# Performance work log

Hardware: AMD Instinct MI355X
Metric: run time of the kernel (lower is better)

## Reference

```python
import jax, jax.numpy as jnp
import numpy as np

BN_EPS = 1e-5

def _conv1x1(x, W, b):
    # x: (B,C,H,W), W: (O,C) -> (B,O,H,W)
    return jnp.einsum('oc,bchw->bohw', W, x) + b[None, :, None, None]

def setup_inputs() -> dict:
    key = jax.random.key(0)
    ks = jax.random.split(key, 6)
    B, C, H, W = 4, 256, 64, 64
    cq = C // 8
    x  = jax.random.normal(ks[0], (B, C, H, W), jnp.float32)
    Wq = jax.random.normal(ks[1], (cq, C), jnp.float32) * (1.0 / np.sqrt(C))
    Wk = jax.random.normal(ks[2], (cq, C), jnp.float32) * (1.0 / np.sqrt(C))
    Wv = jax.random.normal(ks[3], (C, C), jnp.float32) * (1.0 / np.sqrt(C))
    Wo = jax.random.normal(ks[4], (C, C, 3, 3), jnp.float32) * (1.0 / np.sqrt(C * 9))
    return {
        'x': x,
        'Wq': Wq, 'bq': jnp.zeros((cq,), jnp.float32),
        'Wk': Wk, 'bk': jnp.zeros((cq,), jnp.float32),
        'Wv': Wv, 'bv': jnp.zeros((C,), jnp.float32),
        'Wo': Wo, 'bo': jnp.zeros((C,), jnp.float32),
        'bn_gamma': jnp.ones((C,), jnp.float32),
        'bn_beta':  jnp.zeros((C,), jnp.float32),
        'bn_mean':  jnp.zeros((C,), jnp.float32),
        'bn_var':   jnp.ones((C,), jnp.float32),
    }

def reference(x, Wq, bq, Wk, bk, Wv, bv, Wo, bo, bn_gamma, bn_beta, bn_mean, bn_var):
    B, C, H, W = x.shape
    cq = Wq.shape[0]
    N = H * W
    q = _conv1x1(x, Wq, bq).reshape(B, cq, N)   # (B,cq,N)
    k = _conv1x1(x, Wk, bk).reshape(B, cq, N)   # (B,cq,N)
    v = _conv1x1(x, Wv, bv).reshape(B, C, N)    # (B,C,N)
    scale = cq ** (-0.5)
    attn = jnp.einsum('bcn,bcm->bnm', q, k) * scale   # (B,N,N)
    attn = jax.nn.softmax(attn, axis=-1)
    out = jnp.einsum('bnm,bcm->bcn', attn, v).reshape(B, C, H, W)
    # conv_output: 3x3 conv + BN (inference stats) + ReLU
    out = jax.lax.conv_general_dilated(
        out, Wo, window_strides=(1, 1), padding=((1, 1), (1, 1)),
        dimension_numbers=('NCHW', 'OIHW', 'NCHW')) + bo[None, :, None, None]
    inv = bn_gamma * jax.lax.rsqrt(bn_var + BN_EPS)
    out = out * inv[None, :, None, None] + (bn_beta - bn_mean * inv)[None, :, None, None]
    out = jax.nn.relu(out)
    return out + x
```

## Files before the change

### kernel.cpp

```cpp
#include <hip/hip_runtime.h>
#include <hip/hip_bf16.h>
#include <math.h>

#define N_TOK 4096

typedef __attribute__((ext_vector_type(8))) short short8;
typedef __attribute__((ext_vector_type(4))) float f32x4;

#define MFMA16(a, b, c) __builtin_amdgcn_mfma_f32_16x16x32_bf16(a, b, c, 0, 0, 0)

__device__ inline unsigned pack_bf16x2(float a, float b) {
    __hip_bfloat16 ha = __float2bfloat16(a), hb = __float2bfloat16(b);
    unsigned short ua = *(unsigned short*)&ha, ub = *(unsigned short*)&hb;
    return (unsigned)ua | ((unsigned)ub << 16);
}

__device__ inline float bf2f(unsigned short u) {
    unsigned v = ((unsigned)u) << 16;
    union { unsigned u; float f; } cv; cv.u = v; return cv.f;
}

__device__ inline int swz4(int h, int row) { return (h ^ row ^ (row >> 2)) & 3; }

#define SCK 0.25506974748975505f

__global__ __launch_bounds__(256) void xt_prep_kernel(
    const float* __restrict__ x, __hip_bfloat16* __restrict__ xt)
{
    __shared__ __hip_bfloat16 tl[64][72];
    int blk = blockIdx.x;
    int cg = blk & 3, ng = (blk >> 2) & 63, b = blk >> 8;
    int n0 = ng * 64, c0 = cg * 64;
    int t = threadIdx.x;
    int cr = t >> 4, part = t & 15;
#pragma unroll
    for (int rep = 0; rep < 4; ++rep) {
        int c = rep * 16 + cr;
        float4 v4 = *(const float4*)&x[((size_t)(b * 256 + c0 + c)) * N_TOK + n0 + part * 4];
        tl[part * 4 + 0][c] = __float2bfloat16(v4.x);
        tl[part * 4 + 1][c] = __float2bfloat16(v4.y);
        tl[part * 4 + 2][c] = __float2bfloat16(v4.z);
        tl[part * 4 + 3][c] = __float2bfloat16(v4.w);
    }
    __syncthreads();
    int n = t >> 2, g = t & 3;
    uint4 u0 = *(uint4*)&tl[n][g * 16];
    uint4 u1 = *(uint4*)&tl[n][g * 16 + 8];
    __hip_bfloat16* dst = &xt[((size_t)(b * N_TOK + n0 + n)) * 256 + c0 + g * 16];
    *(uint4*)dst = u0;
    *(uint4*)&dst[8] = u1;
}

__global__ __launch_bounds__(256) void w_prep_kernel(
    const float* __restrict__ Wo, const float* __restrict__ Wq,
    const float* __restrict__ Wk, const float* __restrict__ Wv,
    __hip_bfloat16* __restrict__ Wt, __hip_bfloat16* __restrict__ Wqk,
    __hip_bfloat16* __restrict__ Wvb)
{
    int blk = blockIdx.x, t = threadIdx.x;
    if (blk < 256) {
        const float* src = &Wo[(size_t)(blk * 256 + t) * 9];
#pragma unroll
        for (int tap = 0; tap < 9; ++tap)
            Wt[(size_t)(tap * 256 + blk) * 256 + t] = __float2bfloat16(src[tap]);
    } else if (blk < 260) {
        int r0 = (blk - 256) * 64;
        for (int r = r0; r < r0 + 64; ++r)
            Wvb[r * 256 + t] = __float2bfloat16(Wv[r * 256 + t]);
    } else {
        for (int r = 0; r < 32; ++r) {
            Wqk[r * 256 + t]        = __float2bfloat16(Wq[r * 256 + t] * SCK);
            Wqk[(r + 32) * 256 + t] = __float2bfloat16(Wk[r * 256 + t]);
        }
    }
}

__global__ __launch_bounds__(256) void qk_mfma_kernel(
    const __hip_bfloat16* __restrict__ xt, const __hip_bfloat16* __restrict__ Wqk,
    const float* __restrict__ bq, const float* __restrict__ bk,
    __hip_bfloat16* __restrict__ qg, __hip_bfloat16* __restrict__ kg)
{
    int blk = blockIdx.x;
    int b = blk >> 6, n0 = (blk & 63) * 64;
    int t = threadIdx.x, w = t >> 6, lane = t & 63;
    int l15 = lane & 15, l4 = lane >> 4;
    int n = n0 + w * 16 + l15;

    f32x4 zf = {0.f, 0.f, 0.f, 0.f};
    f32x4 acc[4];
#pragma unroll
    for (int m = 0; m < 4; ++m) acc[m] = zf;

    const __hip_bfloat16* xrow = &xt[((size_t)(b * N_TOK + n)) * 256];
    for (int k0 = 0; k0 < 256; k0 += 32) {
        short8 bfr = *(const short8*)&xrow[k0 + l4 * 8];
#pragma unroll
        for (int m = 0; m < 4; ++m) {
            short8 af = *(const short8*)&Wqk[(size_t)(m * 16 + l15) * 256 + k0 + l4 * 8];
            acc[m] = MFMA16(af, bfr, acc[m]);
        }
    }
    f32x4 bq0 = *(const f32x4*)&bq[l4 * 4];
    f32x4 bq1 = *(const f32x4*)&bq[16 + l4 * 4];
    f32x4 bk0 = *(const f32x4*)&bk[l4 * 4];
    f32x4 bk1 = *(const f32x4*)&bk[16 + l4 * 4];
    size_t obase = (size_t)(b * N_TOK + n) * 32;
    uint2 u;
    u.x = pack_bf16x2(acc[0][0] + bq0[0] * SCK, acc[0][1] + bq0[1] * SCK);
    u.y = pack_bf16x2(acc[0][2] + bq0[2] * SCK, acc[0][3] + bq0[3] * SCK);
    *(uint2*)&qg[obase + l4 * 4] = u;
    u.x = pack_bf16x2(acc[1][0] + bq1[0] * SCK, acc[1][1] + bq1[1] * SCK);
    u.y = pack_bf16x2(acc[1][2] + bq1[2] * SCK, acc[1][3] + bq1[3] * SCK);
    *(uint2*)&qg[obase + 16 + l4 * 4] = u;
    u.x = pack_bf16x2(acc[2][0] + bk0[0], acc[2][1] + bk0[1]);
    u.y = pack_bf16x2(acc[2][2] + bk0[2], acc[2][3] + bk0[3]);
    *(uint2*)&kg[obase + l4 * 4] = u;
    u.x = pack_bf16x2(acc[3][0] + bk1[0], acc[3][1] + bk1[1]);
    u.y = pack_bf16x2(acc[3][2] + bk1[2], acc[3][3] + bk1[3]);
    *(uint2*)&kg[obase + 16 + l4 * 4] = u;
}

__global__ __launch_bounds__(256) void v_mfma_kernel(
    const __hip_bfloat16* __restrict__ xt, const __hip_bfloat16* __restrict__ Wvb,
    const float* __restrict__ bv, __hip_bfloat16* __restrict__ vg)
{
    int blk = blockIdx.x;
    int b = blk >> 7, ch = (blk >> 6) & 1, n0 = (blk & 63) * 64;
    int c0 = ch * 128;
    int t = threadIdx.x, w = t >> 6, lane = t & 63;
    int l15 = lane & 15, l4 = lane >> 4;
    int n = n0 + w * 16 + l15;

    f32x4 zf = {0.f, 0.f, 0.f, 0.f};
    f32x4 acc[8];
#pragma unroll
    for (int m = 0; m < 8; ++m) acc[m] = zf;

    const __hip_bfloat16* xrow = &xt[((size_t)(b * N_TOK + n)) * 256];
    for (int k0 = 0; k0 < 256; k0 += 32) {
        short8 bfr = *(const short8*)&xrow[k0 + l4 * 8];
#pragma unroll
        for (int m = 0; m < 8; ++m) {
            short8 af = *(const short8*)&Wvb[(size_t)(c0 + m * 16 + l15) * 256 + k0 + l4 * 8];
            acc[m] = MFMA16(af, bfr, acc[m]);
        }
    }
#pragma unroll
    for (int m = 0; m < 8; ++m) {
        int cb = c0 + m * 16 + l4 * 4;
        f32x4 bvv = *(const f32x4*)&bv[cb];
#pragma unroll
        for (int r = 0; r < 4; ++r)
            vg[((size_t)(b * 256 + cb + r)) * N_TOK + n] = __float2bfloat16(acc[m][r] + bvv[r]);
    }
}

__global__ __launch_bounds__(256, 2) void flash_kernel(
    const __hip_bfloat16* __restrict__ qg, const __hip_bfloat16* __restrict__ kg,
    const __hip_bfloat16* __restrict__ vg,
    __hip_bfloat16* __restrict__ ph0, __hip_bfloat16* __restrict__ ph1,
    float* __restrict__ Lh)
{
    __shared__ __hip_bfloat16 v_lds[2][128 * 64];
    __shared__ __hip_bfloat16 k_lds[2][64 * 32];
    __shared__ __hip_bfloat16 p_lds[4][32 * 64];

    int blk = blockIdx.x;
    int work = (blk & 7) * 64 + (blk >> 3);
    int g = work >> 6;
    int kh = g >> 2, cs = (g >> 1) & 1, bl = g & 1;
    int rem = work & 63;
    int b = ((rem >> 5) << 1) | bl;
    int qgp = rem & 31;
    int t = threadIdx.x, w = t >> 6, lane = t & 63;
    int l15 = lane & 15, l4 = lane >> 4;
    int qw = qgp * 128 + w * 32;

    short8 qf[2];
#pragma unroll
    for (int qs = 0; qs < 2; ++qs)
        qf[qs] = *(const short8*)&qg[((size_t)(b * N_TOK + qw + qs * 16 + l15)) * 32 + l4 * 8];

    f32x4 zf = {0.f, 0.f, 0.f, 0.f};
    f32x4 acc[2][8];
#pragma unroll
    for (int qs = 0; qs < 2; ++qs)
#pragma unroll
        for (int ct = 0; ct < 8; ++ct) acc[qs][ct] = zf;
    float Lr[2] = {0.f, 0.f};

    int vc  = t >> 1;
    int kb4 = (t & 1) * 4;
    int kr  = t >> 2;
    int kch = t & 3;

    const __hip_bfloat16* vrow  = &vg[((size_t)(b * 256 + cs * 128 + vc)) * N_TOK + kh * 2048];
    const __hip_bfloat16* kbase = &kg[((size_t)(b * N_TOK + kh * 2048)) * 32];

    uint4 vp[4], kp;

#pragma unroll
    for (int j = 0; j < 4; ++j)
        vp[j] = *(const uint4*)&vrow[(kb4 + j) * 8];
    kp = *(const uint4*)&kbase[kr * 32 + kch * 8];
#pragma unroll
    for (int j = 0; j < 4; ++j)
        *(uint4*)&v_lds[0][vc * 64 + (((2 * (kb4 + j)) ^ (vc & 14)) << 2)] = vp[j];
    *(uint4*)&k_lds[0][kr * 32 + swz4(kch, kr) * 8] = kp;
    __syncthreads();

    int buf = 0;
    for (int it = 0; it < 32; ++it) {
        int nm0 = it * 64 + 64;
        bool more = (it < 31);
        if (more) {
#pragma unroll
            for (int j = 0; j < 4; ++j)
                vp[j] = *(const uint4*)&vrow[nm0 + (kb4 + j) * 8];
            kp = *(const uint4*)&kbase[(size_t)(nm0 + kr) * 32 + kch * 8];
        }

        short8 kf[4];
#pragma unroll
        for (int kt = 0; kt < 4; ++kt) {
            int row = kt * 16 + l15;
            kf[kt] = *(const short8*)&k_lds[buf][row * 32 + swz4(l4, row) * 8];
        }
        f32x4 sf[2][4];
#pragma unroll
        for (int qs = 0; qs < 2; ++qs)
#pragma unroll
            for (int kt = 0; kt < 4; ++kt)
                sf[qs][kt] = MFMA16(kf[kt], qf[qs], zf);

#pragma unroll
        for (int qs = 0; qs < 2; ++qs) {
            int prow = qs * 16 + l15;
#pragma unroll
            for (int kt = 0; kt < 4; ++kt) {
                float p0 = exp2f(sf[qs][kt][0]);
                float p1 = exp2f(sf[qs][kt][1]);
                float p2 = exp2f(sf[qs][kt][2]);
                float p3 = exp2f(sf[qs][kt][3]);
                Lr[qs] += (p0 + p1) + (p2 + p3);
                uint2 u;
                u.x = pack_bf16x2(p0, p1);
                u.y = pack_bf16x2(p2, p3);
                *(uint2*)&p_lds[w][prow * 64 + (((kt * 4 + l4) ^ (l15 & 14)) << 2)] = u;
            }
        }

#pragma unroll
        for (int ks = 0; ks < 2; ++ks) {
            short8 pb[2];
#pragma unroll
            for (int qs = 0; qs < 2; ++qs)
                pb[qs] = *(const short8*)&p_lds[w][(qs * 16 + l15) * 64 +
                         (((ks * 8 + l4 * 2) ^ (l15 & 14)) << 2)];
#pragma unroll
            for (int ct = 0; ct < 8; ++ct) {
                int cr = ct * 16 + l15;
                short8 vf = *(const short8*)&v_lds[buf][cr * 64 +
                           (((ks * 8 + l4 * 2) ^ (cr & 14)) << 2)];
                acc[0][ct] = MFMA16(vf, pb[0], acc[0][ct]);
                acc[1][ct] = MFMA16(vf, pb[1], acc[1][ct]);
            }
        }

        if (more) {
#pragma unroll
            for (int j = 0; j < 4; ++j)
                *(uint4*)&v_lds[buf ^ 1][vc * 64 + (((2 * (kb4 + j)) ^ (vc & 14)) << 2)] = vp[j];
            *(uint4*)&k_lds[buf ^ 1][kr * 32 + swz4(kch, kr) * 8] = kp;
            buf ^= 1;
        }
        __syncthreads();
    }

#pragma unroll
    for (int qs = 0; qs < 2; ++qs) {
        float L = Lr[qs];
        L += __shfl_xor(L, 16);
        L += __shfl_xor(L, 32);
        int nq = qw + qs * 16 + l15;
        if (cs == 0 && l4 == 0)
            Lh[kh * 16384 + b * 4096 + nq] = L;
        __hip_bfloat16* pdst = kh ? ph1 : ph0;
        size_t pix = (size_t)(b * N_TOK + nq);
#pragma unroll
        for (int ct = 0; ct < 8; ++ct) {
            int cl = cs * 128 + ct * 16 + l4 * 4;
            uint2 u;
            u.x = pack_bf16x2(acc[qs][ct][0], acc[qs][ct][1]);
            u.y = pack_bf16x2(acc[qs][ct][2], acc[qs][ct][3]);
            *(uint2*)&pdst[pix * 256 + cl] = u;
        }
    }
}

__global__ __launch_bounds__(256) void linv_kernel(
    const float* __restrict__ Lh, float* __restrict__ Linv)
{
    int i = blockIdx.x * 256 + threadIdx.x;
    Linv[i] = 1.f / (Lh[i] + Lh[16384 + i]);
}

__global__ __launch_bounds__(256) void conv_mfma_kernel(
    const __hip_bfloat16* __restrict__ ph0, const __hip_bfloat16* __restrict__ ph1,
    const float* __restrict__ Linv, const __hip_bfloat16* __restrict__ Wt,
    const float* __restrict__ bo,  const float* __restrict__ gamma,
    const float* __restrict__ beta, const float* __restrict__ mean,
    const float* __restrict__ var, const float* __restrict__ x,
    float* __restrict__ out)
{
    __shared__ __hip_bfloat16 in_lds[180 * 32];
    __shared__ __hip_bfloat16 wt_lds[9 * 64 * 32];

    int blk = blockIdx.x;
    int sp = blk & 31, ob = (blk >> 5) & 3, b = blk >> 7;
    int y0 = (sp >> 2) * 8, x0 = (sp & 3) * 16;
    int o0 = ob * 64;
    int t = threadIdx.x;
    int w = t >> 6, lane = t & 63;
    int l15 = lane & 15, l4 = lane >> 4;

    f32x4 zf = {0.f, 0.f, 0.f, 0.f};
    f32x4 acc[4][2];
#pragma unroll
    for (int m = 0; m < 4; ++m)
#pragma unroll
        for (int n = 0; n < 2; ++n) acc[m][n] = zf;

    for (int cc = 0; cc < 256; cc += 32) {
        __syncthreads();
        for (int jj = t; jj < 720; jj += 256) {
            int pix = jj >> 2, h = jj & 3;
            int iy = pix / 18, ix = pix - iy * 18;
            int gy = y0 - 1 + iy, gx = x0 - 1 + ix;
            uint4 val = {0u, 0u, 0u, 0u};
            if (gy >= 0 && gy < 64 && gx >= 0 && gx < 64) {
                int bn = b * 4096 + gy * 64 + gx;
                float inv = Linv[bn];
                size_t e = (size_t)bn * 256 + cc + h * 8;
                uint4 a  = *(const uint4*)&ph0[e];
                uint4 b4 = *(const uint4*)&ph1[e];
                const unsigned* ap = (const unsigned*)&a;
                const unsigned* bp = (const unsigned*)&b4;
                unsigned* vpn = (unsigned*)&val;
#pragma unroll
                for (int j = 0; j < 4; ++j) {
                    float lo = (bf2f((unsigned short)(ap[j] & 0xffff)) +
                                bf2f((unsigned short)(bp[j] & 0xffff))) * inv;
                    float hi = (bf2f((unsigned short)(ap[j] >> 16)) +
                                bf2f((unsigned short)(bp[j] >> 16))) * inv;
                    vpn[j] = pack_bf16x2(lo, hi);
                }
            }
            *(uint4*)&in_lds[pix * 32 + swz4(h, pix) * 8] = val;
        }
        for (int jj = t; jj < 2304; jj += 256) {
            int tap = jj >> 8, rem = jj & 255;
            int o = rem >> 2, h = rem & 3;
            uint4 wv = *(const uint4*)&Wt[((size_t)(tap * 256 + o0 + o)) * 256 + cc + h * 8];
            *(uint4*)&wt_lds[tap * 2048 + o * 32 + swz4(h, o) * 8] = wv;
        }
        __syncthreads();

#pragma unroll
        for (int ky = 0; ky < 3; ++ky) {
#pragma unroll
            for (int kx = 0; kx < 3; ++kx) {
                int tap = ky * 3 + kx;
                short8 af[4];
#pragma unroll
                for (int m = 0; m < 4; ++m) {
                    int orow = m * 16 + l15;
                    af[m] = *(const short8*)&wt_lds[tap * 2048 + orow * 32 + swz4(l4, orow) * 8];
                }
#pragma unroll
                for (int ntw = 0; ntw < 2; ++ntw) {
                    int yy = w * 2 + ntw;
                    int p = (yy + ky) * 18 + kx + l15;
                    short8 bfr = *(const short8*)&in_lds[p * 32 + swz4(l4, p) * 8];
#pragma unroll
                    for (int m = 0; m < 4; ++m)
                        acc[m][ntw] = MFMA16(af[m], bfr, acc[m][ntw]);
                }
            }
        }
    }

#pragma unroll
    for (int m = 0; m < 4; ++m) {
#pragma unroll
        for (int r = 0; r < 4; ++r) {
            int oc = o0 + m * 16 + l4 * 4 + r;
            float inv = gamma[oc] * rsqrtf(var[oc] + 1e-5f);
            float sh  = (bo[oc] - mean[oc]) * inv + beta[oc];
#pragma unroll
            for (int ntw = 0; ntw < 2; ++ntw) {
                int gy = y0 + w * 2 + ntw, gx = x0 + l15;
                size_t idx = (size_t)(b * 256 + oc) * 4096 + (size_t)gy * 64 + gx;
                float yv = acc[m][ntw][r] * inv + sh;
                yv = fmaxf(yv, 0.f);
                out[idx] = yv + x[idx];
            }
        }
    }
}

extern "C" void kernel_launch(void* const* d_in, const int* in_sizes, int n_in,
                              void* d_out, int out_size, void* d_ws, size_t ws_size,
                              hipStream_t stream)
{
    const float* x  = (const float*)d_in[0];
    const float* Wq = (const float*)d_in[1];
    const float* bq = (const float*)d_in[2];
    const float* Wk = (const float*)d_in[3];
    const float* bk = (const float*)d_in[4];
    const float* Wv = (const float*)d_in[5];
    const float* bv = (const float*)d_in[6];
    const float* Wo = (const float*)d_in[7];
    const float* bo = (const float*)d_in[8];
    const float* gm = (const float*)d_in[9];
    const float* bt = (const float*)d_in[10];
    const float* mn = (const float*)d_in[11];
    const float* vr = (const float*)d_in[12];
    float* out = (float*)d_out;

    char* wsb = (char*)d_ws;
    __hip_bfloat16* qg  = (__hip_bfloat16*)(wsb);
    __hip_bfloat16* kg  = (__hip_bfloat16*)(wsb + (1u  << 20));
    __hip_bfloat16* vg  = (__hip_bfloat16*)(wsb + (2u  << 20));
    __hip_bfloat16* att = (__hip_bfloat16*)(wsb + (10u << 20));
    __hip_bfloat16* Wt  = (__hip_bfloat16*)(wsb + (18u << 20));
    __hip_bfloat16* xt  = (__hip_bfloat16*)(wsb + (20u << 20));
    __hip_bfloat16* Wqk = (__hip_bfloat16*)(wsb + (28u << 20));
    __hip_bfloat16* Wvb = (__hip_bfloat16*)(wsb + (28u << 20) + 65536);
    float*          Lh  = (float*)(wsb + (28u << 20) + 262144);
    float*          Linv= (float*)(wsb + (28u << 20) + 393216);

    __hip_bfloat16* ph0 = xt;
    __hip_bfloat16* ph1 = att;

    w_prep_kernel  <<<261,  256, 0, stream>>>(Wo, Wq, Wk, Wv, Wt, Wqk, Wvb);
    xt_prep_kernel <<<1024, 256, 0, stream>>>(x, xt);
    qk_mfma_kernel <<<256,  256, 0, stream>>>(xt, Wqk, bq, bk, qg, kg);
    v_mfma_kernel  <<<512,  256, 0, stream>>>(xt, Wvb, bv, vg);
    flash_kernel   <<<512,  256, 0, stream>>>(qg, kg, vg, ph0, ph1, Lh);
    linv_kernel    <<<64,   256, 0, stream>>>(Lh, Linv);
    conv_mfma_kernel<<<512, 256, 0, stream>>>(ph0, ph1, Linv, Wt, bo, gm, bt, mn, vr, x, out);
}
```

Before: 160.6 us.

## Split flash attention keys three ways and load K fragments directly into registers

```diff
diff --git a/kernel.cpp b/kernel.cpp
--- a/kernel.cpp
+++ b/kernel.cpp
@@ -155,23 +155,22 @@
     }
 }
 
-__global__ __launch_bounds__(256, 2) void flash_kernel(
+__global__ __launch_bounds__(256, 3) void flash_kernel(
     const __hip_bfloat16* __restrict__ qg, const __hip_bfloat16* __restrict__ kg,
     const __hip_bfloat16* __restrict__ vg,
     __hip_bfloat16* __restrict__ ph0, __hip_bfloat16* __restrict__ ph1,
-    float* __restrict__ Lh)
+    __hip_bfloat16* __restrict__ ph2, float* __restrict__ Lh)
 {
     __shared__ __hip_bfloat16 v_lds[2][128 * 64];
-    __shared__ __hip_bfloat16 k_lds[2][64 * 32];
     __shared__ __hip_bfloat16 p_lds[4][32 * 64];
 
     int blk = blockIdx.x;
-    int work = (blk & 7) * 64 + (blk >> 3);
-    int g = work >> 6;
-    int kh = g >> 2, cs = (g >> 1) & 1, bl = g & 1;
-    int rem = work & 63;
-    int b = ((rem >> 5) << 1) | bl;
-    int qgp = rem & 31;
+    int work = (blk & 7) * 96 + (blk >> 3);
+    int kh = work >> 8;
+    int rem = work & 255;
+    int cs = rem >> 7, b = (rem >> 5) & 3, qgp = rem & 31;
+    int koff  = (kh == 0) ? 0 : (kh == 1 ? 1408 : 2752);
+    int iters = (kh == 0) ? 22 : 21;
     int t = threadIdx.x, w = t >> 6, lane = t & 63;
     int l15 = lane & 15, l4 = lane >> 4;
     int qw = qgp * 128 + w * 32;
@@ -191,47 +190,43 @@
 
     int vc  = t >> 1;
     int kb4 = (t & 1) * 4;
-    int kr  = t >> 2;
-    int kch = t & 3;
-
-    const __hip_bfloat16* vrow  = &vg[((size_t)(b * 256 + cs * 128 + vc)) * N_TOK + kh * 2048];
-    const __hip_bfloat16* kbase = &kg[((size_t)(b * N_TOK + kh * 2048)) * 32];
-
-    uint4 vp[4], kp;
+
+    const __hip_bfloat16* vrow  = &vg[((size_t)(b * 256 + cs * 128 + vc)) * N_TOK + koff];
+    const __hip_bfloat16* kbase = &kg[((size_t)(b * N_TOK + koff)) * 32];
+
+    uint4 vp[4];
+    short8 kfr[4], kfn[4];
 
 #pragma unroll
     for (int j = 0; j < 4; ++j)
         vp[j] = *(const uint4*)&vrow[(kb4 + j) * 8];
-    kp = *(const uint4*)&kbase[kr * 32 + kch * 8];
+#pragma unroll
+    for (int kt = 0; kt < 4; ++kt)
+        kfr[kt] = *(const short8*)&kbase[(kt * 16 + l15) * 32 + l4 * 8];
 #pragma unroll
     for (int j = 0; j < 4; ++j)
         *(uint4*)&v_lds[0][vc * 64 + (((2 * (kb4 + j)) ^ (vc & 14)) << 2)] = vp[j];
-    *(uint4*)&k_lds[0][kr * 32 + swz4(kch, kr) * 8] = kp;
     __syncthreads();
 
     int buf = 0;
-    for (int it = 0; it < 32; ++it) {
+    for (int it = 0; it < iters; ++it) {
         int nm0 = it * 64 + 64;
-        bool more = (it < 31);
+        bool more = (it < iters - 1);
         if (more) {
 #pragma unroll
             for (int j = 0; j < 4; ++j)
                 vp[j] = *(const uint4*)&vrow[nm0 + (kb4 + j) * 8];
-            kp = *(const uint4*)&kbase[(size_t)(nm0 + kr) * 32 + kch * 8];
-        }
-
-        short8 kf[4];
-#pragma unroll
-        for (int kt = 0; kt < 4; ++kt) {
-            int row = kt * 16 + l15;
-            kf[kt] = *(const short8*)&k_lds[buf][row * 32 + swz4(l4, row) * 8];
-        }
+#pragma unroll
+            for (int kt = 0; kt < 4; ++kt)
+                kfn[kt] = *(const short8*)&kbase[(size_t)(nm0 + kt * 16 + l15) * 32 + l4 * 8];
+        }
+
         f32x4 sf[2][4];
 #pragma unroll
         for (int qs = 0; qs < 2; ++qs)
 #pragma unroll
             for (int kt = 0; kt < 4; ++kt)
-                sf[qs][kt] = MFMA16(kf[kt], qf[qs], zf);
+                sf[qs][kt] = MFMA16(kfr[kt], qf[qs], zf);
 
 #pragma unroll
         for (int qs = 0; qs < 2; ++qs) {
@@ -271,7 +266,8 @@
 #pragma unroll
             for (int j = 0; j < 4; ++j)
                 *(uint4*)&v_lds[buf ^ 1][vc * 64 + (((2 * (kb4 + j)) ^ (vc & 14)) << 2)] = vp[j];
-            *(uint4*)&k_lds[buf ^ 1][kr * 32 + swz4(kch, kr) * 8] = kp;
+#pragma unroll
+            for (int kt = 0; kt < 4; ++kt) kfr[kt] = kfn[kt];
             buf ^= 1;
         }
         __syncthreads();
@@ -285,7 +281,7 @@
         int nq = qw + qs * 16 + l15;
         if (cs == 0 && l4 == 0)
             Lh[kh * 16384 + b * 4096 + nq] = L;
-        __hip_bfloat16* pdst = kh ? ph1 : ph0;
+        __hip_bfloat16* pdst = (kh == 0) ? ph0 : (kh == 1 ? ph1 : ph2);
         size_t pix = (size_t)(b * N_TOK + nq);
 #pragma unroll
         for (int ct = 0; ct < 8; ++ct) {
@@ -302,12 +298,13 @@
     const float* __restrict__ Lh, float* __restrict__ Linv)
 {
     int i = blockIdx.x * 256 + threadIdx.x;
-    Linv[i] = 1.f / (Lh[i] + Lh[16384 + i]);
+    Linv[i] = 1.f / (Lh[i] + Lh[16384 + i] + Lh[32768 + i]);
 }
 
 __global__ __launch_bounds__(256) void conv_mfma_kernel(
     const __hip_bfloat16* __restrict__ ph0, const __hip_bfloat16* __restrict__ ph1,
-    const float* __restrict__ Linv, const __hip_bfloat16* __restrict__ Wt,
+    const __hip_bfloat16* __restrict__ ph2, const float* __restrict__ Linv,
+    const __hip_bfloat16* __restrict__ Wt,
     const float* __restrict__ bo,  const float* __restrict__ gamma,
     const float* __restrict__ beta, const float* __restrict__ mean,
     const float* __restrict__ var, const float* __restrict__ x,
@@ -344,15 +341,19 @@
                 size_t e = (size_t)bn * 256 + cc + h * 8;
                 uint4 a  = *(const uint4*)&ph0[e];
                 uint4 b4 = *(const uint4*)&ph1[e];
+                uint4 c4 = *(const uint4*)&ph2[e];
                 const unsigned* ap = (const unsigned*)&a;
                 const unsigned* bp = (const unsigned*)&b4;
+                const unsigned* cp = (const unsigned*)&c4;
                 unsigned* vpn = (unsigned*)&val;
 #pragma unroll
                 for (int j = 0; j < 4; ++j) {
                     float lo = (bf2f((unsigned short)(ap[j] & 0xffff)) +
-                                bf2f((unsigned short)(bp[j] & 0xffff))) * inv;
+                                bf2f((unsigned short)(bp[j] & 0xffff)) +
+                                bf2f((unsigned short)(cp[j] & 0xffff))) * inv;
                     float hi = (bf2f((unsigned short)(ap[j] >> 16)) +
-                                bf2f((unsigned short)(bp[j] >> 16))) * inv;
+                                bf2f((unsigned short)(bp[j] >> 16)) +
+                                bf2f((unsigned short)(cp[j] >> 16))) * inv;
                     vpn[j] = pack_bf16x2(lo, hi);
                 }
             }
@@ -438,7 +439,8 @@
     __hip_bfloat16* Wqk = (__hip_bfloat16*)(wsb + (28u << 20));
     __hip_bfloat16* Wvb = (__hip_bfloat16*)(wsb + (28u << 20) + 65536);
     float*          Lh  = (float*)(wsb + (28u << 20) + 262144);
-    float*          Linv= (float*)(wsb + (28u << 20) + 393216);
+    float*          Linv= (float*)(wsb + (28u << 20) + 458752);
+    __hip_bfloat16* ph2 = (__hip_bfloat16*)(wsb + (29u << 20));
 
     __hip_bfloat16* ph0 = xt;
     __hip_bfloat16* ph1 = att;
@@ -447,7 +449,7 @@
     xt_prep_kernel <<<1024, 256, 0, stream>>>(x, xt);
     qk_mfma_kernel <<<256,  256, 0, stream>>>(xt, Wqk, bq, bk, qg, kg);
     v_mfma_kernel  <<<512,  256, 0, stream>>>(xt, Wvb, bv, vg);
-    flash_kernel   <<<512,  256, 0, stream>>>(qg, kg, vg, ph0, ph1, Lh);
+    flash_kernel   <<<768,  256, 0, stream>>>(qg, kg, vg, ph0, ph1, ph2, Lh);
     linv_kernel    <<<64,   256, 0, stream>>>(Lh, Linv);
-    conv_mfma_kernel<<<512, 256, 0, stream>>>(ph0, ph1, Linv, Wt, bo, gm, bt, mn, vr, x, out);
-}
+    conv_mfma_kernel<<<512, 256, 0, stream>>>(ph0, ph1, ph2, Linv, Wt, bo, gm, bt, mn, vr, x, out);
+}
```

Measured after the change: 179.0 us. 11.4% more time.

## Fuse x transpose, QK and V projections into one kernel; inline L reciprocal

Applied to the files above, without the earlier changes.

```diff
diff --git a/kernel.cpp b/kernel.cpp
--- a/kernel.cpp
+++ b/kernel.cpp
@@ -23,33 +23,6 @@
 __device__ inline int swz4(int h, int row) { return (h ^ row ^ (row >> 2)) & 3; }
 
 #define SCK 0.25506974748975505f
-
-__global__ __launch_bounds__(256) void xt_prep_kernel(
-    const float* __restrict__ x, __hip_bfloat16* __restrict__ xt)
-{
-    __shared__ __hip_bfloat16 tl[64][72];
-    int blk = blockIdx.x;
-    int cg = blk & 3, ng = (blk >> 2) & 63, b = blk >> 8;
-    int n0 = ng * 64, c0 = cg * 64;
-    int t = threadIdx.x;
-    int cr = t >> 4, part = t & 15;
-#pragma unroll
-    for (int rep = 0; rep < 4; ++rep) {
-        int c = rep * 16 + cr;
-        float4 v4 = *(const float4*)&x[((size_t)(b * 256 + c0 + c)) * N_TOK + n0 + part * 4];
-        tl[part * 4 + 0][c] = __float2bfloat16(v4.x);
-        tl[part * 4 + 1][c] = __float2bfloat16(v4.y);
-        tl[part * 4 + 2][c] = __float2bfloat16(v4.z);
-        tl[part * 4 + 3][c] = __float2bfloat16(v4.w);
-    }
-    __syncthreads();
-    int n = t >> 2, g = t & 3;
-    uint4 u0 = *(uint4*)&tl[n][g * 16];
-    uint4 u1 = *(uint4*)&tl[n][g * 16 + 8];
-    __hip_bfloat16* dst = &xt[((size_t)(b * N_TOK + n0 + n)) * 256 + c0 + g * 16];
-    *(uint4*)dst = u0;
-    *(uint4*)&dst[8] = u1;
-}
 
 __global__ __launch_bounds__(256) void w_prep_kernel(
     const float* __restrict__ Wo, const float* __restrict__ Wq,
@@ -75,11 +48,15 @@
     }
 }
 
-__global__ __launch_bounds__(256) void qk_mfma_kernel(
-    const __hip_bfloat16* __restrict__ xt, const __hip_bfloat16* __restrict__ Wqk,
+__global__ __launch_bounds__(256) void qkv_kernel(
+    const float* __restrict__ x,
+    const __hip_bfloat16* __restrict__ Wqk, const __hip_bfloat16* __restrict__ Wvb,
     const float* __restrict__ bq, const float* __restrict__ bk,
-    __hip_bfloat16* __restrict__ qg, __hip_bfloat16* __restrict__ kg)
+    const float* __restrict__ bv,
+    __hip_bfloat16* __restrict__ qg, __hip_bfloat16* __restrict__ kg,
+    __hip_bfloat16* __restrict__ vg)
 {
+    __shared__ __hip_bfloat16 tl[64][72];
     int blk = blockIdx.x;
     int b = blk >> 6, n0 = (blk & 63) * 64;
     int t = threadIdx.x, w = t >> 6, lane = t & 63;
@@ -87,71 +64,69 @@
     int n = n0 + w * 16 + l15;
 
     f32x4 zf = {0.f, 0.f, 0.f, 0.f};
-    f32x4 acc[4];
-#pragma unroll
-    for (int m = 0; m < 4; ++m) acc[m] = zf;
-
-    const __hip_bfloat16* xrow = &xt[((size_t)(b * N_TOK + n)) * 256];
-    for (int k0 = 0; k0 < 256; k0 += 32) {
-        short8 bfr = *(const short8*)&xrow[k0 + l4 * 8];
-#pragma unroll
-        for (int m = 0; m < 4; ++m) {
-            short8 af = *(const short8*)&Wqk[(size_t)(m * 16 + l15) * 256 + k0 + l4 * 8];
-            acc[m] = MFMA16(af, bfr, acc[m]);
-        }
-    }
+    f32x4 aqk[4], av[16];
+#pragma unroll
+    for (int m = 0; m < 4; ++m) aqk[m] = zf;
+#pragma unroll
+    for (int m = 0; m < 16; ++m) av[m] = zf;
+
+    int cr = t >> 4, part = t & 15;
+
+    for (int cc = 0; cc < 256; cc += 64) {
+        __syncthreads();
+#pragma unroll
+        for (int rep = 0; rep < 4; ++rep) {
+            int c = rep * 16 + cr;
+            float4 v4 = *(const float4*)&x[((size_t)(b * 256 + cc + c)) * N_TOK + n0 + part * 4];
+            tl[part * 4 + 0][c] = __float2bfloat16(v4.x);
+            tl[part * 4 + 1][c] = __float2bfloat16(v4.y);
+            tl[part * 4 + 2][c] = __float2bfloat16(v4.z);
+            tl[part * 4 + 3][c] = __float2bfloat16(v4.w);
+        }
+        __syncthreads();
+#pragma unroll
+        for (int kk = 0; kk < 2; ++kk) {
+            int k0 = cc + kk * 32;
+            short8 bfr = *(const short8*)&tl[w * 16 + l15][kk * 32 + l4 * 8];
+#pragma unroll
+            for (int m = 0; m < 4; ++m) {
+                short8 af = *(const short8*)&Wqk[(size_t)(m * 16 + l15) * 256 + k0 + l4 * 8];
+                aqk[m] = MFMA16(af, bfr, aqk[m]);
+            }
+#pragma unroll
+            for (int m = 0; m < 16; ++m) {
+                short8 af = *(const short8*)&Wvb[(size_t)(m * 16 + l15) * 256 + k0 + l4 * 8];
+                av[m] = MFMA16(af, bfr, av[m]);
+            }
+        }
+    }
+
     f32x4 bq0 = *(const f32x4*)&bq[l4 * 4];
     f32x4 bq1 = *(const f32x4*)&bq[16 + l4 * 4];
     f32x4 bk0 = *(const f32x4*)&bk[l4 * 4];
     f32x4 bk1 = *(const f32x4*)&bk[16 + l4 * 4];
     size_t obase = (size_t)(b * N_TOK + n) * 32;
     uint2 u;
-    u.x = pack_bf16x2(acc[0][0] + bq0[0] * SCK, acc[0][1] + bq0[1] * SCK);
-    u.y = pack_bf16x2(acc[0][2] + bq0[2] * SCK, acc[0][3] + bq0[3] * SCK);
+    u.x = pack_bf16x2(aqk[0][0] + bq0[0] * SCK, aqk[0][1] + bq0[1] * SCK);
+    u.y = pack_bf16x2(aqk[0][2] + bq0[2] * SCK, aqk[0][3] + bq0[3] * SCK);
     *(uint2*)&qg[obase + l4 * 4] = u;
-    u.x = pack_bf16x2(acc[1][0] + bq1[0] * SCK, acc[1][1] + bq1[1] * SCK);
-    u.y = pack_bf16x2(acc[1][2] + bq1[2] * SCK, acc[1][3] + bq1[3] * SCK);
+    u.x = pack_bf16x2(aqk[1][0] + bq1[0] * SCK, aqk[1][1] + bq1[1] * SCK);
+    u.y = pack_bf16x2(aqk[1][2] + bq1[2] * SCK, aqk[1][3] + bq1[3] * SCK);
     *(uint2*)&qg[obase + 16 + l4 * 4] = u;
-    u.x = pack_bf16x2(acc[2][0] + bk0[0], acc[2][1] + bk0[1]);
-    u.y = pack_bf16x2(acc[2][2] + bk0[2], acc[2][3] + bk0[3]);
+    u.x = pack_bf16x2(aqk[2][0] + bk0[0], aqk[2][1] + bk0[1]);
+    u.y = pack_bf16x2(aqk[2][2] + bk0[2], aqk[2][3] + bk0[3]);
     *(uint2*)&kg[obase + l4 * 4] = u;
-    u.x = pack_bf16x2(acc[3][0] + bk1[0], acc[3][1] + bk1[1]);
-    u.y = pack_bf16x2(acc[3][2] + bk1[2], acc[3][3] + bk1[3]);
+    u.x = pack_bf16x2(aqk[3][0] + bk1[0], aqk[3][1] + bk1[1]);
+    u.y = pack_bf16x2(aqk[3][2] + bk1[2], aqk[3][3] + bk1[3]);
     *(uint2*)&kg[obase + 16 + l4 * 4] = u;
-}
-
-__global__ __launch_bounds__(256) void v_mfma_kernel(
-    const __hip_bfloat16* __restrict__ xt, const __hip_bfloat16* __restrict__ Wvb,
-    const float* __restrict__ bv, __hip_bfloat16* __restrict__ vg)
-{
-    int blk = blockIdx.x;
-    int b = blk >> 7, ch = (blk >> 6) & 1, n0 = (blk & 63) * 64;
-    int c0 = ch * 128;
-    int t = threadIdx.x, w = t >> 6, lane = t & 63;
-    int l15 = lane & 15, l4 = lane >> 4;
-    int n = n0 + w * 16 + l15;
-
-    f32x4 zf = {0.f, 0.f, 0.f, 0.f};
-    f32x4 acc[8];
-#pragma unroll
-    for (int m = 0; m < 8; ++m) acc[m] = zf;
-
-    const __hip_bfloat16* xrow = &xt[((size_t)(b * N_TOK + n)) * 256];
-    for (int k0 = 0; k0 < 256; k0 += 32) {
-        short8 bfr = *(const short8*)&xrow[k0 + l4 * 8];
-#pragma unroll
-        for (int m = 0; m < 8; ++m) {
-            short8 af = *(const short8*)&Wvb[(size_t)(c0 + m * 16 + l15) * 256 + k0 + l4 * 8];
-            acc[m] = MFMA16(af, bfr, acc[m]);
-        }
-    }
-#pragma unroll
-    for (int m = 0; m < 8; ++m) {
-        int cb = c0 + m * 16 + l4 * 4;
+
+#pragma unroll
+    for (int m = 0; m < 16; ++m) {
+        int cb = m * 16 + l4 * 4;
         f32x4 bvv = *(const f32x4*)&bv[cb];
 #pragma unroll
         for (int r = 0; r < 4; ++r)
-            vg[((size_t)(b * 256 + cb + r)) * N_TOK + n] = __float2bfloat16(acc[m][r] + bvv[r]);
+            vg[((size_t)(b * 256 + cb + r)) * N_TOK + n] = __float2bfloat16(av[m][r] + bvv[r]);
     }
 }
 
@@ -298,16 +273,9 @@
     }
 }
 
-__global__ __launch_bounds__(256) void linv_kernel(
-    const float* __restrict__ Lh, float* __restrict__ Linv)
-{
-    int i = blockIdx.x * 256 + threadIdx.x;
-    Linv[i] = 1.f / (Lh[i] + Lh[16384 + i]);
-}
-
 __global__ __launch_bounds__(256) void conv_mfma_kernel(
     const __hip_bfloat16* __restrict__ ph0, const __hip_bfloat16* __restrict__ ph1,
-    const float* __restrict__ Linv, const __hip_bfloat16* __restrict__ Wt,
+    const float* __restrict__ Lh, const __hip_bfloat16* __restrict__ Wt,
     const float* __restrict__ bo,  const float* __restrict__ gamma,
     const float* __restrict__ beta, const float* __restrict__ mean,
     const float* __restrict__ var, const float* __restrict__ x,
@@ -340,7 +308,7 @@
             uint4 val = {0u, 0u, 0u, 0u};
             if (gy >= 0 && gy < 64 && gx >= 0 && gx < 64) {
                 int bn = b * 4096 + gy * 64 + gx;
-                float inv = Linv[bn];
+                float inv = 1.f / (Lh[bn] + Lh[16384 + bn]);
                 size_t e = (size_t)bn * 256 + cc + h * 8;
                 uint4 a  = *(const uint4*)&ph0[e];
                 uint4 b4 = *(const uint4*)&ph1[e];
@@ -432,22 +400,15 @@
     __hip_bfloat16* qg  = (__hip_bfloat16*)(wsb);
     __hip_bfloat16* kg  = (__hip_bfloat16*)(wsb + (1u  << 20));
     __hip_bfloat16* vg  = (__hip_bfloat16*)(wsb + (2u  << 20));
-    __hip_bfloat16* att = (__hip_bfloat16*)(wsb + (10u << 20));
+    __hip_bfloat16* ph1 = (__hip_bfloat16*)(wsb + (10u << 20));
     __hip_bfloat16* Wt  = (__hip_bfloat16*)(wsb + (18u << 20));
-    __hip_bfloat16* xt  = (__hip_bfloat16*)(wsb + (20u << 20));
+    __hip_bfloat16* ph0 = (__hip_bfloat16*)(wsb + (20u << 20));
     __hip_bfloat16* Wqk = (__hip_bfloat16*)(wsb + (28u << 20));
     __hip_bfloat16* Wvb = (__hip_bfloat16*)(wsb + (28u << 20) + 65536);
     float*          Lh  = (float*)(wsb + (28u << 20) + 262144);
-    float*          Linv= (float*)(wsb + (28u << 20) + 393216);
-
-    __hip_bfloat16* ph0 = xt;
-    __hip_bfloat16* ph1 = att;
 
     w_prep_kernel  <<<261,  256, 0, stream>>>(Wo, Wq, Wk, Wv, Wt, Wqk, Wvb);
-    xt_prep_kernel <<<1024, 256, 0, stream>>>(x, xt);
-    qk_mfma_kernel <<<256,  256, 0, stream>>>(xt, Wqk, bq, bk, qg, kg);
-    v_mfma_kernel  <<<512,  256, 0, stream>>>(xt, Wvb, bv, vg);
+    qkv_kernel     <<<256,  256, 0, stream>>>(x, Wqk, Wvb, bq, bk, bv, qg, kg, vg);
     flash_kernel   <<<512,  256, 0, stream>>>(qg, kg, vg, ph0, ph1, Lh);
-    linv_kernel    <<<64,   256, 0, stream>>>(Lh, Linv);
-    conv_mfma_kernel<<<512, 256, 0, stream>>>(ph0, ph1, Linv, Wt, bo, gm, bt, mn, vr, x, out);
-}
+    conv_mfma_kernel<<<512, 256, 0, stream>>>(ph0, ph1, Lh, Wt, bo, gm, bt, mn, vr, x, out);
+}
```

Result: faster. 155.2 us (-3.3%).
